# Kernel tuning notes

Measured on AMD Instinct MI355X. Metric: run time of the kernel, lower is better.

The kernel has to match this reference:

```python
import jax, jax.numpy as jnp
import numpy as np

B, C_IN, V_IN = 16, 16, 16000
V1, V2 = 16384, 4096          # V2 = V1 // 4 (after first pool)
K1, K2 = 16, 16               # Chebyshev orders
F1, F2 = 32, 64               # conv output channels
FC1_F = 512
DEG = 16
EPS = 1e-5


def setup_inputs() -> dict:
    key = jax.random.key(0)
    ks = jax.random.split(key, 12)
    x = jax.random.normal(ks[0], (B, C_IN, V_IN), dtype=jnp.float32)
    perm_idx = jax.random.permutation(ks[1], V1).astype(jnp.int32)
    # sparse rescaled Laplacians in COO form (row, col, val)
    l1_rows = jnp.repeat(jnp.arange(V1, dtype=jnp.int32), DEG)
    l1_cols = jax.random.randint(ks[2], (V1 * DEG,), 0, V1, dtype=jnp.int32)
    l1_vals = jax.random.normal(ks[3], (V1 * DEG,), dtype=jnp.float32) / DEG
    l2_rows = jnp.repeat(jnp.arange(V2, dtype=jnp.int32), DEG)
    l2_cols = jax.random.randint(ks[4], (V2 * DEG,), 0, V2, dtype=jnp.int32)
    l2_vals = jax.random.normal(ks[5], (V2 * DEG,), dtype=jnp.float32) / DEG
    # Graph_Conv kernels: Linear(in_channels*K -> out_channels)
    s1 = np.sqrt(2.0 / (C_IN * K1 + F1)).astype(np.float32)
    w1 = jax.random.uniform(ks[6], (F1, C_IN * K1), jnp.float32, -s1, s1)
    b1 = jnp.zeros((F1,), jnp.float32)
    s2 = np.sqrt(2.0 / (F1 * K2 + F2)).astype(np.float32)
    w2 = jax.random.uniform(ks[7], (F2, F1 * K2), jnp.float32, -s2, s2)
    b2 = jnp.zeros((F2,), jnp.float32)
    fc_in = F2 * (V1 // 16)  # 65536
    s3 = np.sqrt(2.0 / (fc_in + FC1_F)).astype(np.float32)
    fc1_w = jax.random.uniform(ks[8], (FC1_F, fc_in), jnp.float32, -s3, s3)
    fc1_b = jnp.zeros((FC1_F,), jnp.float32)
    return dict(x=x, perm_idx=perm_idx,
                l1_rows=l1_rows, l1_cols=l1_cols, l1_vals=l1_vals,
                l2_rows=l2_rows, l2_cols=l2_cols, l2_vals=l2_vals,
                w1=w1, b1=b1, w2=w2, b2=b2, fc1_w=fc1_w, fc1_b=fc1_b)


def _spmm(rows, cols, vals, X, V):
    # sparse (V,V) @ dense (V,M) via gather + segment-sum
    return jax.ops.segment_sum(vals[:, None] * X[cols], rows, num_segments=V)


def _cheb_conv(x, rows, cols, vals, w, b, K):
    # x: (B, C, V) -> (B, Fout, V)
    Bn, C, V = x.shape
    x0 = x.transpose(2, 1, 0).reshape(V, C * Bn)
    xs = [x0]
    if K > 1:
        xs.append(_spmm(rows, cols, vals, x0, V))
    for _ in range(2, K):
        xs.append(2.0 * _spmm(rows, cols, vals, xs[-1], V) - xs[-2])
    xk = jnp.stack(xs, axis=0).reshape(K, V, C, Bn)    # (K, V, C, B)
    xk = xk.transpose(3, 1, 2, 0).reshape(Bn * V, C * K)
    y = xk @ w.T + b                                   # (B*V, Fout)
    return y.reshape(Bn, V, -1).transpose(0, 2, 1)     # (B, Fout, V)


def _pool4(x):
    Bn, C, V = x.shape
    return x.reshape(Bn, C, V // 4, 4).max(axis=-1)


def reference(x, perm_idx, l1_rows, l1_cols, l1_vals,
              l2_rows, l2_cols, l2_vals,
              w1, b1, w2, b2, fc1_w, fc1_b):
    # BatchNorm1d(affine=False), training-mode (batch) statistics
    mean = x.mean(axis=(0, 2), keepdims=True)
    var = x.var(axis=(0, 2), keepdims=True)
    x = (x - mean) * jax.lax.rsqrt(var + EPS)
    # Permute: zero-pad vertices to V1, then reorder
    Bn, C, V = x.shape
    x = jnp.pad(x, ((0, 0), (0, 0), (0, V1 - V)))[:, :, perm_idx]
    # conv1 -> relu -> pool4
    x = jax.nn.relu(_cheb_conv(x, l1_rows, l1_cols, l1_vals, w1, b1, K1))
    x = _pool4(x)
    # conv2 -> relu -> pool4
    x = jax.nn.relu(_cheb_conv(x, l2_rows, l2_cols, l2_vals, w2, b2, K2))
    x = _pool4(x)
    # flatten + fc1 (dropout is identity in eval mode)
    x = x.reshape(Bn, -1)
    return x @ fc1_w.T + fc1_b
```

## Files before the change

### kernel.cpp

```cpp
#include <hip/hip_runtime.h>

#define VIN  16000
#define V1q  16384
#define V2q  4096
#define Kq   16
#define F1q  32
#define F2q  64
#define FCIN 65536

typedef unsigned short u16;
typedef __attribute__((ext_vector_type(8))) short short8;
typedef __attribute__((ext_vector_type(4))) float f32x4;

__device__ __forceinline__ float bf2f(u16 v) { return __uint_as_float((unsigned)v << 16); }
__device__ __forceinline__ u16 f2bf(float f) {
    unsigned u = __float_as_uint(f);
    return (u16)((u + 0x7fffu + ((u >> 16) & 1u)) >> 16);
}

__global__ void bn_part(const float* __restrict__ x, float* __restrict__ part) {
    int c  = blockIdx.y;
    int bx = blockIdx.x;
    int b  = bx >> 2;
    int vc = bx & 3;
    const float* p = x + (size_t)(b * 16 + c) * VIN + vc * 4000;
    float s = 0.f, s2 = 0.f;
    for (int v = threadIdx.x; v < 4000; v += 256) {
        float val = p[v];
        s += val; s2 += val * val;
    }
    for (int o = 32; o; o >>= 1) { s += __shfl_down(s, o); s2 += __shfl_down(s2, o); }
    __shared__ float ls[4], ls2[4];
    int wid = threadIdx.x >> 6;
    if ((threadIdx.x & 63) == 0) { ls[wid] = s; ls2[wid] = s2; }
    __syncthreads();
    if (threadIdx.x == 0) {
        s = ls[0] + ls[1] + ls[2] + ls[3];
        s2 = ls2[0] + ls2[1] + ls2[2] + ls2[3];
        part[(c * 64 + bx) * 2]     = s;
        part[(c * 64 + bx) * 2 + 1] = s2;
    }
}

__global__ void bn_final(const float* __restrict__ part, float* __restrict__ mean_rstd) {
    int t = threadIdx.x;
    int c = t >> 4, j = t & 15;
    float s = 0.f, s2 = 0.f;
    for (int i = 0; i < 4; i++) {
        s  += part[(c * 64 + j * 4 + i) * 2];
        s2 += part[(c * 64 + j * 4 + i) * 2 + 1];
    }
    for (int o = 8; o; o >>= 1) { s += __shfl_down(s, o, 16); s2 += __shfl_down(s2, o, 16); }
    if (j == 0) {
        float m  = s / 256000.f;
        float var = s2 / 256000.f - m * m;
        mean_rstd[c]      = m;
        mean_rstd[16 + c] = rsqrtf(var + 1e-5f);
    }
}

__global__ void build_iperm(const int* __restrict__ perm, int* __restrict__ iperm) {
    int v = blockIdx.x * 256 + threadIdx.x;
    if (v < V1q) iperm[perm[v]] = v;
}

__global__ void norm_transpose_scatter(const float* __restrict__ x,
                                       const float* __restrict__ mean_rstd,
                                       const int* __restrict__ iperm,
                                       u16* __restrict__ X0) {
    __shared__ u16 tile[256][33];
    int u0 = blockIdx.x * 32;
    int t  = threadIdx.x;
    int jj = t & 31, half = t >> 5;
    for (int rr = 0; rr < 32; rr++) {
        int s = rr * 8 + half;
        int c = s & 15, b = s >> 4;
        float val = x[(size_t)s * VIN + u0 + jj];
        val = (val - mean_rstd[c]) * mean_rstd[16 + c];
        int d = ((c >> 3) << 7) | (b << 3) | (c & 7);
        tile[d][jj] = f2bf(val);
    }
    __syncthreads();
    for (int j = 0; j < 32; j++) {
        int tv = iperm[u0 + j];
        X0[(size_t)tv * 256 + t] = tile[t][j];
    }
}

__global__ void pack_w1(const float* __restrict__ w1, u16* __restrict__ B1p) {
    int i = blockIdx.x * 256 + threadIdx.x;
    int j = i & 7, l = (i >> 3) & 63, nf = (i >> 9) & 1, s = i >> 10;
    int q = l >> 4;
    int k = s * 2 + (q >> 1);
    int c = (q & 1) * 8 + j;
    int f = nf * 16 + (l & 15);
    B1p[i] = f2bf(w1[f * 256 + c * 16 + k]);
}
__global__ void pack_w2(const float* __restrict__ w2, u16* __restrict__ B2p) {
    int i = blockIdx.x * 256 + threadIdx.x;
    int j = i & 7, l = (i >> 3) & 63, nf = (i >> 9) & 3, k = i >> 11;
    int f1 = (l >> 4) * 8 + j;
    int f2 = nf * 16 + (l & 15);
    B2p[i] = f2bf(w2[f2 * 512 + f1 * 16 + k]);
}

__global__ void pack_p(const float* __restrict__ P2f, u16* __restrict__ Pp) {
    int i = blockIdx.x * 256 + threadIdx.x;
    int l = i & 63, ks = i >> 6;
    int b = l & 15, q = l >> 4;
    const float* src = P2f + (size_t)b * FCIN + ks * 32 + q * 8;
    float4 a0 = *(const float4*)(src);
    float4 a1 = *(const float4*)(src + 4);
    short8 v;
    v[0] = (short)f2bf(a0.x); v[1] = (short)f2bf(a0.y);
    v[2] = (short)f2bf(a0.z); v[3] = (short)f2bf(a0.w);
    v[4] = (short)f2bf(a1.x); v[5] = (short)f2bf(a1.y);
    v[6] = (short)f2bf(a1.z); v[7] = (short)f2bf(a1.w);
    *(short8*)(Pp + (size_t)i * 8) = v;
}

template<int WLOG, int NRBLOG>
__global__ void spmm_cheb(const u16* __restrict__ prev, const u16* __restrict__ prev2,
                          u16* __restrict__ out,
                          const int* __restrict__ cols, const float* __restrict__ vals,
                          int nwg, float scale, int sub) {
    int bid = blockIdx.x;
    int q = nwg >> 3;
    int wid = (bid & 7) * q + (bid >> 3);
    int cb = wid >> NRBLOG;
    int r4 = wid & ((1 << NRBLOG) - 1);
    int lane = threadIdx.x & 63;
    int r = __builtin_amdgcn_readfirstlane(r4 * 4 + (threadIdx.x >> 6));
    int col = (cb << 6) + lane;
    const int4*   cp = (const int4*)(cols + r * 16);
    const float4* vp = (const float4*)(vals + r * 16);
    float acc = 0.f;
#pragma unroll
    for (int ii = 0; ii < 4; ii++) {
        int4   ci = cp[ii];
        float4 vi = vp[ii];
        const u16* p0 = prev + ((size_t)__builtin_amdgcn_readfirstlane(ci.x) << WLOG);
        const u16* p1 = prev + ((size_t)__builtin_amdgcn_readfirstlane(ci.y) << WLOG);
        const u16* p2 = prev + ((size_t)__builtin_amdgcn_readfirstlane(ci.z) << WLOG);
        const u16* p3 = prev + ((size_t)__builtin_amdgcn_readfirstlane(ci.w) << WLOG);
        acc += vi.x * bf2f(p0[col]);
        acc += vi.y * bf2f(p1[col]);
        acc += vi.z * bf2f(p2[col]);
        acc += vi.w * bf2f(p3[col]);
    }
    float o = scale * acc;
    if (sub) o -= bf2f(__builtin_nontemporal_load(prev2 + ((size_t)r << WLOG) + col));
    __builtin_nontemporal_store(f2bf(o), out + ((size_t)r << WLOG) + col);
}

__launch_bounds__(256)
__global__ void gemm1_mfma(const u16* __restrict__ XS1, const u16* __restrict__ B1p,
                           const float* __restrict__ b1, u16* __restrict__ XS2_0) {
    __shared__ u16 As[2][4096];
    int t = threadIdx.x;
    int w = t >> 6, l = t & 63;
    int v0 = blockIdx.x * 8;
    int nf = w & 1, vq = w >> 1;

    f32x4 acc[4] = {};
    {
        const short8* s0 = (const short8*)(XS1 + (size_t)(0 * V1q + v0) * 256);
        const short8* s1 = (const short8*)(XS1 + (size_t)(1 * V1q + v0) * 256);
        short8* dst = (short8*)As[0];
        dst[t] = s0[t]; dst[256 + t] = s1[t];
    }
    __syncthreads();
    for (int s = 0; s < 8; s++) {
        int cur = s & 1;
        if (s < 7) {
            const short8* s0 = (const short8*)(XS1 + (size_t)((2 * s + 2) * V1q + v0) * 256);
            const short8* s1 = (const short8*)(XS1 + (size_t)((2 * s + 3) * V1q + v0) * 256);
            short8* dst = (short8*)As[cur ^ 1];
            dst[t] = s0[t]; dst[256 + t] = s1[t];
        }
        short8 bfrag = *(const short8*)(B1p + (((size_t)s * 2 + nf) * 64 + l) * 8);
        int abase = (l >> 5) * 2048 + (l & 31) * 8;
#pragma unroll
        for (int fm = 0; fm < 4; fm++) {
            int vl = vq * 4 + fm;
            short8 afrag = *(const short8*)&As[cur][abase + vl * 256];
            acc[fm] = __builtin_amdgcn_mfma_f32_16x16x32_bf16(afrag, bfrag, acc[fm], 0, 0, 0);
        }
        __syncthreads();
    }
    f32x4 m = acc[0];
#pragma unroll
    for (int fm = 1; fm < 4; fm++) {
#pragma unroll
        for (int i = 0; i < 4; i++) m[i] = fmaxf(m[i], acc[fm][i]);
    }
    int f1 = nf * 16 + (l & 15);
    float bias = b1[f1];
    int u_out = blockIdx.x * 2 + vq;
    u16* orow = XS2_0 + (size_t)u_out * 512;
    int colbase = ((f1 >> 3) << 7) | (f1 & 7);
#pragma unroll
    for (int reg = 0; reg < 4; reg++) {
        int b = (l >> 4) * 4 + reg;
        orow[colbase + b * 8] = f2bf(fmaxf(m[reg] + bias, 0.f));
    }
}

__launch_bounds__(256)
__global__ void gemm2_mfma(const u16* __restrict__ XS2, const u16* __restrict__ B2p,
                           const float* __restrict__ b2, float* __restrict__ P2f) {
    __shared__ u16 As[2][8192];
    __shared__ float ylds[4 * 16 * 66];
    int t = threadIdx.x;
    int w = t >> 6, l = t & 63;
    int u0 = blockIdx.x * 16;

    f32x4 acc[4][4] = {};
    {
        const short8* src = (const short8*)(XS2 + (size_t)(0 * V2q + u0) * 512);
        short8* dst = (short8*)As[0];
#pragma unroll
        for (int r = 0; r < 4; r++) dst[t * 4 + r] = src[t * 4 + r];
    }
    __syncthreads();
    for (int k = 0; k < 16; k++) {
        int cur = k & 1;
        if (k < 15) {
            const short8* src = (const short8*)(XS2 + (size_t)((k + 1) * V2q + u0) * 512);
            short8* dst = (short8*)As[cur ^ 1];
#pragma unroll
            for (int r = 0; r < 4; r++) dst[t * 4 + r] = src[t * 4 + r];
        }
        short8 bfrag[4];
#pragma unroll
        for (int nf = 0; nf < 4; nf++)
            bfrag[nf] = *(const short8*)(B2p + (((size_t)k * 4 + nf) * 64 + l) * 8);
#pragma unroll
        for (int fm = 0; fm < 4; fm++) {
            int ul = w * 4 + fm;
            short8 afrag = *(const short8*)&As[cur][ul * 512 + l * 8];
#pragma unroll
            for (int nf = 0; nf < 4; nf++)
                acc[fm][nf] = __builtin_amdgcn_mfma_f32_16x16x32_bf16(afrag, bfrag[nf], acc[fm][nf], 0, 0, 0);
        }
        __syncthreads();
    }
#pragma unroll
    for (int nf = 0; nf < 4; nf++) {
        int f2 = nf * 16 + (l & 15);
        float bias = b2[f2];
#pragma unroll
        for (int reg = 0; reg < 4; reg++) {
            int b = (l >> 4) * 4 + reg;
            float m = fmaxf(fmaxf(acc[0][nf][reg], acc[1][nf][reg]),
                            fmaxf(acc[2][nf][reg], acc[3][nf][reg]));
            ylds[(w * 16 + b) * 66 + f2] = fmaxf(m + bias, 0.f);
        }
    }
    __syncthreads();
    int ub = blockIdx.x * 4;
#pragma unroll
    for (int i = 0; i < 4; i++) {
        int p = t + i * 256;
        int b = p >> 6, f2 = p & 63;
        float4 v;
        v.x = ylds[(0 * 16 + b) * 66 + f2];
        v.y = ylds[(1 * 16 + b) * 66 + f2];
        v.z = ylds[(2 * 16 + b) * 66 + f2];
        v.w = ylds[(3 * 16 + b) * 66 + f2];
        *(float4*)&P2f[(size_t)(b * 64 + f2) * 1024 + ub] = v;
    }
}

__global__ void fc_init(const float* __restrict__ b, float* __restrict__ out) {
    int i = blockIdx.x * 256 + threadIdx.x;
    out[i] = b[i & 511];
}

__launch_bounds__(256)
__global__ void fc_mfma(const u16* __restrict__ Pp, const float* __restrict__ W,
                        float* __restrict__ out) {
    int t = threadIdx.x;
    int w = t >> 6, l = t & 63;
    int n0 = blockIdx.x * 16;
    int ks0 = blockIdx.y * 64 + w * 16;
    int o = n0 + (l & 15);
    const float* wp = W + (size_t)o * FCIN + (size_t)ks0 * 32 + (l >> 4) * 8;
    const u16*   ap = Pp + ((size_t)ks0 * 64 + l) * 8;
    f32x4 acc = {};
    for (int s = 0; s < 16; s++) {
        short8 afrag = *(const short8*)(ap + (size_t)s * 512);
        float4 w0 = *(const float4*)(wp + s * 32);
        float4 w1 = *(const float4*)(wp + s * 32 + 4);
        short8 bfrag;
        bfrag[0] = (short)f2bf(w0.x); bfrag[1] = (short)f2bf(w0.y);
        bfrag[2] = (short)f2bf(w0.z); bfrag[3] = (short)f2bf(w0.w);
        bfrag[4] = (short)f2bf(w1.x); bfrag[5] = (short)f2bf(w1.y);
        bfrag[6] = (short)f2bf(w1.z); bfrag[7] = (short)f2bf(w1.w);
        acc = __builtin_amdgcn_mfma_f32_16x16x32_bf16(afrag, bfrag, acc, 0, 0, 0);
    }
    __shared__ float red[4][256];
#pragma unroll
    for (int r = 0; r < 4; r++)
        red[w][((l >> 4) * 4 + r) * 16 + (l & 15)] = acc[r];
    __syncthreads();
    float s = red[0][t] + red[1][t] + red[2][t] + red[3][t];
    atomicAdd(&out[(t >> 4) * 512 + n0 + (t & 15)], s);
}

extern "C" void kernel_launch(void* const* d_in, const int* in_sizes, int n_in,
                              void* d_out, int out_size, void* d_ws, size_t ws_size,
                              hipStream_t stream) {
    const float* x       = (const float*)d_in[0];
    const int*   perm    = (const int*)d_in[1];
    const int*   l1_cols = (const int*)d_in[3];
    const float* l1_vals = (const float*)d_in[4];
    const int*   l2_cols = (const int*)d_in[6];
    const float* l2_vals = (const float*)d_in[7];
    const float* w1      = (const float*)d_in[8];
    const float* b1      = (const float*)d_in[9];
    const float* w2      = (const float*)d_in[10];
    const float* b2      = (const float*)d_in[11];
    const float* fcw     = (const float*)d_in[12];
    const float* fcb     = (const float*)d_in[13];
    float* out = (float*)d_out;

    char* wsb = (char*)d_ws;
    size_t off = 0;
    auto alloc = [&](size_t bytes) -> void* {
        void* p = wsb + off;
        off += (bytes + 255) & ~(size_t)255;
        return p;
    };
    float* mean_rstd = (float*)alloc(32 * 4);
    float* bnpart    = (float*)alloc(16 * 64 * 2 * 4);
    int*   iperm     = (int*)alloc((size_t)V1q * 4);
    u16*   B1p       = (u16*)alloc(8192 * 2);
    u16*   B2p       = (u16*)alloc(32768 * 2);
    u16*   XS1       = (u16*)alloc((size_t)Kq * V1q * 256 * 2);
    u16*   XS2       = (u16*)alloc((size_t)Kq * V2q * 512 * 2);
    float* P2f       = (float*)alloc((size_t)16 * FCIN * 4);
    u16*   Pp        = (u16*)alloc((size_t)16 * FCIN * 2);
    (void)ws_size; (void)in_sizes; (void)n_in; (void)out_size;

    const size_t S1 = (size_t)V1q * 256;
    const size_t S2 = (size_t)V2q * 512;

    bn_part<<<dim3(64, 16), 256, 0, stream>>>(x, bnpart);
    bn_final<<<1, 256, 0, stream>>>(bnpart, mean_rstd);
    build_iperm<<<V1q / 256, 256, 0, stream>>>(perm, iperm);
    hipMemsetAsync(XS1, 0, S1 * 2, stream);
    norm_transpose_scatter<<<500, 256, 0, stream>>>(x, mean_rstd, iperm, XS1);
    pack_w1<<<32, 256, 0, stream>>>(w1, B1p);
    pack_w2<<<128, 256, 0, stream>>>(w2, B2p);

    spmm_cheb<8, 12><<<16384, 256, 0, stream>>>(XS1, XS1, XS1 + S1, l1_cols, l1_vals, 16384, 1.f, 0);
    for (int k = 2; k < Kq; k++)
        spmm_cheb<8, 12><<<16384, 256, 0, stream>>>(XS1 + (size_t)(k - 1) * S1, XS1 + (size_t)(k - 2) * S1,
                                                    XS1 + (size_t)k * S1, l1_cols, l1_vals, 16384, 2.f, 1);
    gemm1_mfma<<<V1q / 8, 256, 0, stream>>>(XS1, B1p, b1, XS2);

    spmm_cheb<9, 10><<<8192, 256, 0, stream>>>(XS2, XS2, XS2 + S2, l2_cols, l2_vals, 8192, 1.f, 0);
    for (int k = 2; k < Kq; k++)
        spmm_cheb<9, 10><<<8192, 256, 0, stream>>>(XS2 + (size_t)(k - 1) * S2, XS2 + (size_t)(k - 2) * S2,
                                                   XS2 + (size_t)k * S2, l2_cols, l2_vals, 8192, 2.f, 1);
    gemm2_mfma<<<V2q / 16, 256, 0, stream>>>(XS2, B2p, b2, P2f);

    pack_p<<<512, 256, 0, stream>>>(P2f, Pp);
    fc_init<<<32, 256, 0, stream>>>(fcb, out);
    fc_mfma<<<dim3(32, 32), 256, 0, stream>>>(Pp, fcw, out);
}
```

Baseline: 481.0 us.

## Restructure Chebyshev SpMM so each wave processes whole rows with vector loads

Replaces the column-block SpMM, where one wave handled a 64-column slice of a row with 2-byte loads, with a row-per-wave kernel. Each lane now loads 4 or 8 packed bf16 values per neighbor, so the column/value indices are read once per full row instead of once per column block. Fewer, larger blocks loop over rows. The hipMemsetAsync is also replaced with a custom zeroing kernel. In exchange, per-wave load size and register use rise, and the cross-block L2-locality swizzle of the old scheme is dropped.

Result: faster. 464.4 us (-3.4%).

```diff
diff --git a/kernel.cpp b/kernel.cpp
--- a/kernel.cpp
+++ b/kernel.cpp
@@ -4,18 +4,30 @@
 #define V1q  16384
 #define V2q  4096
 #define Kq   16
-#define F1q  32
-#define F2q  64
 #define FCIN 65536
 
 typedef unsigned short u16;
+typedef unsigned int u32;
 typedef __attribute__((ext_vector_type(8))) short short8;
 typedef __attribute__((ext_vector_type(4))) float f32x4;
+typedef __attribute__((ext_vector_type(2))) u32 u32x2;
+typedef __attribute__((ext_vector_type(4))) u32 u32x4;
 
 __device__ __forceinline__ float bf2f(u16 v) { return __uint_as_float((unsigned)v << 16); }
+__device__ __forceinline__ float bflo(u32 u) { return __uint_as_float(u << 16); }
+__device__ __forceinline__ float bfhi(u32 u) { return __uint_as_float(u & 0xffff0000u); }
 __device__ __forceinline__ u16 f2bf(float f) {
     unsigned u = __float_as_uint(f);
     return (u16)((u + 0x7fffu + ((u >> 16) & 1u)) >> 16);
+}
+__device__ __forceinline__ u32 packbf(float a, float b) {
+    return (u32)f2bf(a) | ((u32)f2bf(b) << 16);
+}
+
+__global__ void zero_ws(u16* __restrict__ X0) {
+    size_t idx = (size_t)blockIdx.x * 256 + threadIdx.x;
+    float4 z = {0.f, 0.f, 0.f, 0.f};
+    *(float4*)(X0 + idx * 8) = z;
 }
 
 __global__ void bn_part(const float* __restrict__ x, float* __restrict__ part) {
@@ -119,38 +131,75 @@
     *(short8*)(Pp + (size_t)i * 8) = v;
 }
 
-template<int WLOG, int NRBLOG>
-__global__ void spmm_cheb(const u16* __restrict__ prev, const u16* __restrict__ prev2,
-                          u16* __restrict__ out,
-                          const int* __restrict__ cols, const float* __restrict__ vals,
-                          int nwg, float scale, int sub) {
-    int bid = blockIdx.x;
-    int q = nwg >> 3;
-    int wid = (bid & 7) * q + (bid >> 3);
-    int cb = wid >> NRBLOG;
-    int r4 = wid & ((1 << NRBLOG) - 1);
+template<int CPL>
+__launch_bounds__(256)
+__global__ void spmm_row(const u16* __restrict__ prev, const u16* __restrict__ prev2,
+                         u16* __restrict__ out,
+                         const int* __restrict__ cols, const float* __restrict__ vals,
+                         int iters, float scale, int sub) {
+    constexpr int WLOG = (CPL == 2) ? 8 : 9;
+    constexpr int EPL  = CPL * 2;
     int lane = threadIdx.x & 63;
-    int r = __builtin_amdgcn_readfirstlane(r4 * 4 + (threadIdx.x >> 6));
-    int col = (cb << 6) + lane;
-    const int4*   cp = (const int4*)(cols + r * 16);
-    const float4* vp = (const float4*)(vals + r * 16);
-    float acc = 0.f;
-#pragma unroll
-    for (int ii = 0; ii < 4; ii++) {
-        int4   ci = cp[ii];
-        float4 vi = vp[ii];
-        const u16* p0 = prev + ((size_t)__builtin_amdgcn_readfirstlane(ci.x) << WLOG);
-        const u16* p1 = prev + ((size_t)__builtin_amdgcn_readfirstlane(ci.y) << WLOG);
-        const u16* p2 = prev + ((size_t)__builtin_amdgcn_readfirstlane(ci.z) << WLOG);
-        const u16* p3 = prev + ((size_t)__builtin_amdgcn_readfirstlane(ci.w) << WLOG);
-        acc += vi.x * bf2f(p0[col]);
-        acc += vi.y * bf2f(p1[col]);
-        acc += vi.z * bf2f(p2[col]);
-        acc += vi.w * bf2f(p3[col]);
-    }
-    float o = scale * acc;
-    if (sub) o -= bf2f(__builtin_nontemporal_load(prev2 + ((size_t)r << WLOG) + col));
-    __builtin_nontemporal_store(f2bf(o), out + ((size_t)r << WLOG) + col);
+    int gw = blockIdx.x * 4 + (threadIdx.x >> 6);
+    int rbase = gw * iters;
+    for (int it = 0; it < iters; it++) {
+        int r = __builtin_amdgcn_readfirstlane(rbase + it);
+        const int4*   cp = (const int4*)(cols + r * 16);
+        const float4* vp = (const float4*)(vals + r * 16);
+        float acc[EPL];
+#pragma unroll
+        for (int i = 0; i < EPL; i++) acc[i] = 0.f;
+#pragma unroll
+        for (int ii = 0; ii < 4; ii++) {
+            int4   ci = cp[ii];
+            float4 vi = vp[ii];
+            int   cs[4] = {ci.x, ci.y, ci.z, ci.w};
+            float vs[4] = {vi.x, vi.y, vi.z, vi.w};
+#pragma unroll
+            for (int j = 0; j < 4; j++) {
+                const u16* rowp = prev + ((size_t)__builtin_amdgcn_readfirstlane(cs[j]) << WLOG);
+                if constexpr (CPL == 2) {
+                    u32x2 g = *(const u32x2*)(rowp + lane * 4);
+                    acc[0] += vs[j] * bflo(g.x); acc[1] += vs[j] * bfhi(g.x);
+                    acc[2] += vs[j] * bflo(g.y); acc[3] += vs[j] * bfhi(g.y);
+                } else {
+                    u32x4 g = *(const u32x4*)(rowp + lane * 8);
+                    acc[0] += vs[j] * bflo(g.x); acc[1] += vs[j] * bfhi(g.x);
+                    acc[2] += vs[j] * bflo(g.y); acc[3] += vs[j] * bfhi(g.y);
+                    acc[4] += vs[j] * bflo(g.z); acc[5] += vs[j] * bfhi(g.z);
+                    acc[6] += vs[j] * bflo(g.w); acc[7] += vs[j] * bfhi(g.w);
+                }
+            }
+        }
+        size_t obase = ((size_t)r << WLOG) + lane * EPL;
+        float o[EPL];
+        if (sub) {
+            if constexpr (CPL == 2) {
+                u32x2 p2 = __builtin_nontemporal_load((const u32x2*)(prev2 + obase));
+                o[0] = scale * acc[0] - bflo(p2.x); o[1] = scale * acc[1] - bfhi(p2.x);
+                o[2] = scale * acc[2] - bflo(p2.y); o[3] = scale * acc[3] - bfhi(p2.y);
+            } else {
+                u32x4 p2 = __builtin_nontemporal_load((const u32x4*)(prev2 + obase));
+                o[0] = scale * acc[0] - bflo(p2.x); o[1] = scale * acc[1] - bfhi(p2.x);
+                o[2] = scale * acc[2] - bflo(p2.y); o[3] = scale * acc[3] - bfhi(p2.y);
+                o[4] = scale * acc[4] - bflo(p2.z); o[5] = scale * acc[5] - bfhi(p2.z);
+                o[6] = scale * acc[6] - bflo(p2.w); o[7] = scale * acc[7] - bfhi(p2.w);
+            }
+        } else {
+#pragma unroll
+            for (int i = 0; i < EPL; i++) o[i] = scale * acc[i];
+        }
+        if constexpr (CPL == 2) {
+            u32x2 pk;
+            pk.x = packbf(o[0], o[1]); pk.y = packbf(o[2], o[3]);
+            __builtin_nontemporal_store(pk, (u32x2*)(out + obase));
+        } else {
+            u32x4 pk;
+            pk.x = packbf(o[0], o[1]); pk.y = packbf(o[2], o[3]);
+            pk.z = packbf(o[4], o[5]); pk.w = packbf(o[6], o[7]);
+            __builtin_nontemporal_store(pk, (u32x4*)(out + obase));
+        }
+    }
 }
 
 __launch_bounds__(256)
@@ -346,24 +395,24 @@
     const size_t S1 = (size_t)V1q * 256;
     const size_t S2 = (size_t)V2q * 512;
 
+    zero_ws<<<2048, 256, 0, stream>>>(XS1);
     bn_part<<<dim3(64, 16), 256, 0, stream>>>(x, bnpart);
     bn_final<<<1, 256, 0, stream>>>(bnpart, mean_rstd);
     build_iperm<<<V1q / 256, 256, 0, stream>>>(perm, iperm);
-    hipMemsetAsync(XS1, 0, S1 * 2, stream);
     norm_transpose_scatter<<<500, 256, 0, stream>>>(x, mean_rstd, iperm, XS1);
     pack_w1<<<32, 256, 0, stream>>>(w1, B1p);
     pack_w2<<<128, 256, 0, stream>>>(w2, B2p);
 
-    spmm_cheb<8, 12><<<16384, 256, 0, stream>>>(XS1, XS1, XS1 + S1, l1_cols, l1_vals, 16384, 1.f, 0);
+    spmm_row<2><<<2048, 256, 0, stream>>>(XS1, XS1, XS1 + S1, l1_cols, l1_vals, 2, 1.f, 0);
     for (int k = 2; k < Kq; k++)
-        spmm_cheb<8, 12><<<16384, 256, 0, stream>>>(XS1 + (size_t)(k - 1) * S1, XS1 + (size_t)(k - 2) * S1,
-                                                    XS1 + (size_t)k * S1, l1_cols, l1_vals, 16384, 2.f, 1);
+        spmm_row<2><<<2048, 256, 0, stream>>>(XS1 + (size_t)(k - 1) * S1, XS1 + (size_t)(k - 2) * S1,
+                                              XS1 + (size_t)k * S1, l1_cols, l1_vals, 2, 2.f, 1);
     gemm1_mfma<<<V1q / 8, 256, 0, stream>>>(XS1, B1p, b1, XS2);
 
-    spmm_cheb<9, 10><<<8192, 256, 0, stream>>>(XS2, XS2, XS2 + S2, l2_cols, l2_vals, 8192, 1.f, 0);
+    spmm_row<4><<<1024, 256, 0, stream>>>(XS2, XS2, XS2 + S2, l2_cols, l2_vals, 1, 1.f, 0);
     for (int k = 2; k < Kq; k++)
-        spmm_cheb<9, 10><<<8192, 256, 0, stream>>>(XS2 + (size_t)(k - 1) * S2, XS2 + (size_t)(k - 2) * S2,
-                                                   XS2 + (size_t)k * S2, l2_cols, l2_vals, 8192, 2.f, 1);
+        spmm_row<4><<<1024, 256, 0, stream>>>(XS2 + (size_t)(k - 1) * S2, XS2 + (size_t)(k - 2) * S2,
+                                              XS2 + (size_t)k * S2, l2_cols, l2_vals, 1, 2.f, 1);
     gemm2_mfma<<<V2q / 16, 256, 0, stream>>>(XS2, B2p, b2, P2f);
 
     pack_p<<<512, 256, 0, stream>>>(P2f, Pp);
```

## Fuse Chebyshev SpMM recurrence into one persistent kernel with grid barriers

Applied to the files above, without the earlier changes.

Replaces the 15 separate spmm_cheb launches per conv layer with a single persistent cheb_chain kernel of 512 workgroups. Each workgroup handles several rows and loops over all Chebyshev orders. Between orders, workgroups sync through a hierarchical per-XCD atomic grid barrier, which is meant to remove kernel launch and drain overhead. The memset is also replaced by a custom zeroing kernel. Correctness depends on every workgroup being co-resident, since the barrier deadlocks otherwise. Fewer waves are in flight to hide gather latency.

Result: slower. 893.0 us (+85.6%).

```diff
diff --git a/kernel.cpp b/kernel.cpp
--- a/kernel.cpp
+++ b/kernel.cpp
@@ -4,11 +4,10 @@
 #define V1q  16384
 #define V2q  4096
 #define Kq   16
-#define F1q  32
-#define F2q  64
 #define FCIN 65536
 
 typedef unsigned short u16;
+typedef unsigned int u32;
 typedef __attribute__((ext_vector_type(8))) short short8;
 typedef __attribute__((ext_vector_type(4))) float f32x4;
 
@@ -16,6 +15,25 @@
 __device__ __forceinline__ u16 f2bf(float f) {
     unsigned u = __float_as_uint(f);
     return (u16)((u + 0x7fffu + ((u >> 16) & 1u)) >> 16);
+}
+
+#define BO_XCNT 0
+#define BO_ARR0 512
+#define BO_FLG0 544
+#define BO_XARR 1024
+#define BO_DONE 9216
+#define BO_FLAG 9984
+#define BAR_CH  16384
+
+__global__ void zero_bar(int* __restrict__ bar) {
+    int i = blockIdx.x * 256 + threadIdx.x;
+    bar[i] = 0;
+}
+
+__global__ void zero_ws(u16* __restrict__ X0) {
+    size_t idx = (size_t)blockIdx.x * 256 + threadIdx.x;
+    float4 z = {0.f, 0.f, 0.f, 0.f};
+    *(float4*)(X0 + idx * 8) = z;
 }
 
 __global__ void bn_part(const float* __restrict__ x, float* __restrict__ part) {
@@ -119,38 +137,84 @@
     *(short8*)(Pp + (size_t)i * 8) = v;
 }
 
-template<int WLOG, int NRBLOG>
-__global__ void spmm_cheb(const u16* __restrict__ prev, const u16* __restrict__ prev2,
-                          u16* __restrict__ out,
-                          const int* __restrict__ cols, const float* __restrict__ vals,
-                          int nwg, float scale, int sub) {
-    int bid = blockIdx.x;
-    int q = nwg >> 3;
-    int wid = (bid & 7) * q + (bid >> 3);
-    int cb = wid >> NRBLOG;
-    int r4 = wid & ((1 << NRBLOG) - 1);
+template<int WLOG, int CBLOG, int NR>
+__launch_bounds__(256, 2)
+__global__ void cheb_chain(const int* __restrict__ cols, const float* __restrict__ vals,
+                           u16* __restrict__ XS, int* __restrict__ bar, size_t S) {
+    int wid = blockIdx.x;
+    int cb  = wid & ((1 << CBLOG) - 1);
+    int rg  = wid >> CBLOG;
     int lane = threadIdx.x & 63;
-    int r = __builtin_amdgcn_readfirstlane(r4 * 4 + (threadIdx.x >> 6));
-    int col = (cb << 6) + lane;
-    const int4*   cp = (const int4*)(cols + r * 16);
-    const float4* vp = (const float4*)(vals + r * 16);
-    float acc = 0.f;
-#pragma unroll
-    for (int ii = 0; ii < 4; ii++) {
-        int4   ci = cp[ii];
-        float4 vi = vp[ii];
-        const u16* p0 = prev + ((size_t)__builtin_amdgcn_readfirstlane(ci.x) << WLOG);
-        const u16* p1 = prev + ((size_t)__builtin_amdgcn_readfirstlane(ci.y) << WLOG);
-        const u16* p2 = prev + ((size_t)__builtin_amdgcn_readfirstlane(ci.z) << WLOG);
-        const u16* p3 = prev + ((size_t)__builtin_amdgcn_readfirstlane(ci.w) << WLOG);
-        acc += vi.x * bf2f(p0[col]);
-        acc += vi.y * bf2f(p1[col]);
-        acc += vi.z * bf2f(p2[col]);
-        acc += vi.w * bf2f(p3[col]);
-    }
-    float o = scale * acc;
-    if (sub) o -= bf2f(__builtin_nontemporal_load(prev2 + ((size_t)r << WLOG) + col));
-    __builtin_nontemporal_store(f2bf(o), out + ((size_t)r << WLOG) + col);
+    int wv   = __builtin_amdgcn_readfirstlane(threadIdx.x >> 6);
+    int col  = (cb << 6) + lane;
+    int rbase = (rg * 4 + wv) * NR;
+    int nwg = gridDim.x;
+
+    int myxcd;
+    asm volatile("s_getreg_b32 %0, hwreg(HW_REG_XCC_ID)" : "=s"(myxcd));
+    myxcd &= 15;
+
+    int mycount = 0, nxcd = 0;
+    if (threadIdx.x == 0) {
+        __hip_atomic_fetch_add(&bar[BO_XCNT + myxcd * 32], 1, __ATOMIC_RELAXED, __HIP_MEMORY_SCOPE_AGENT);
+        int prev = __hip_atomic_fetch_add(&bar[BO_ARR0], 1, __ATOMIC_RELEASE, __HIP_MEMORY_SCOPE_AGENT);
+        if (prev == nwg - 1) {
+            __hip_atomic_store(&bar[BO_FLG0], 1, __ATOMIC_RELEASE, __HIP_MEMORY_SCOPE_AGENT);
+        } else {
+            while (__hip_atomic_load(&bar[BO_FLG0], __ATOMIC_RELAXED, __HIP_MEMORY_SCOPE_AGENT) == 0)
+                __builtin_amdgcn_s_sleep(4);
+        }
+        mycount = __hip_atomic_load(&bar[BO_XCNT + myxcd * 32], __ATOMIC_RELAXED, __HIP_MEMORY_SCOPE_AGENT);
+        for (int j = 0; j < 16; j++)
+            nxcd += (__hip_atomic_load(&bar[BO_XCNT + j * 32], __ATOMIC_RELAXED, __HIP_MEMORY_SCOPE_AGENT) != 0);
+    }
+    __syncthreads();
+    asm volatile("" ::: "memory");
+
+    for (int k = 1; k < 16; k++) {
+        const u16* prev  = XS + (size_t)(k - 1) * S;
+        const u16* prev2 = XS + (size_t)(k - 2) * S;
+        u16* outp = XS + (size_t)k * S;
+        float scale = (k == 1) ? 1.f : 2.f;
+#pragma unroll 2
+        for (int it = 0; it < NR; it++) {
+            int r = __builtin_amdgcn_readfirstlane(rbase + it);
+            const int4*   cp = (const int4*)(cols + r * 16);
+            const float4* vp = (const float4*)(vals + r * 16);
+            float acc = 0.f;
+#pragma unroll
+            for (int ii = 0; ii < 4; ii++) {
+                int4   ci = cp[ii];
+                float4 vi = vp[ii];
+                acc += vi.x * bf2f(prev[((size_t)__builtin_amdgcn_readfirstlane(ci.x) << WLOG) + col]);
+                acc += vi.y * bf2f(prev[((size_t)__builtin_amdgcn_readfirstlane(ci.y) << WLOG) + col]);
+                acc += vi.z * bf2f(prev[((size_t)__builtin_amdgcn_readfirstlane(ci.z) << WLOG) + col]);
+                acc += vi.w * bf2f(prev[((size_t)__builtin_amdgcn_readfirstlane(ci.w) << WLOG) + col]);
+            }
+            size_t ob = ((size_t)r << WLOG) + col;
+            float o = scale * acc;
+            if (k >= 2) o -= bf2f(__builtin_nontemporal_load(prev2 + ob));
+            outp[ob] = f2bf(o);
+        }
+        if (k < 15) {
+            __syncthreads();
+            if (threadIdx.x == 0) {
+                int xa = __hip_atomic_fetch_add(&bar[BO_XARR + (k * 16 + myxcd) * 32], 1,
+                                                __ATOMIC_RELAXED, __HIP_MEMORY_SCOPE_AGENT);
+                if (xa == mycount - 1) {
+                    __builtin_amdgcn_fence(__ATOMIC_RELEASE, "agent");
+                    int d = __hip_atomic_fetch_add(&bar[BO_DONE + k * 32], 1,
+                                                   __ATOMIC_RELEASE, __HIP_MEMORY_SCOPE_AGENT);
+                    if (d == nxcd - 1)
+                        __hip_atomic_store(&bar[BO_FLAG], k, __ATOMIC_RELEASE, __HIP_MEMORY_SCOPE_AGENT);
+                }
+                while (__hip_atomic_load(&bar[BO_FLAG], __ATOMIC_RELAXED, __HIP_MEMORY_SCOPE_AGENT) < k)
+                    __builtin_amdgcn_s_sleep(4);
+            }
+            __syncthreads();
+            asm volatile("" ::: "memory");
+        }
+    }
 }
 
 __launch_bounds__(256)
@@ -335,6 +399,7 @@
     float* mean_rstd = (float*)alloc(32 * 4);
     float* bnpart    = (float*)alloc(16 * 64 * 2 * 4);
     int*   iperm     = (int*)alloc((size_t)V1q * 4);
+    int*   bar       = (int*)alloc((size_t)2 * BAR_CH * 4);
     u16*   B1p       = (u16*)alloc(8192 * 2);
     u16*   B2p       = (u16*)alloc(32768 * 2);
     u16*   XS1       = (u16*)alloc((size_t)Kq * V1q * 256 * 2);
@@ -346,24 +411,18 @@
     const size_t S1 = (size_t)V1q * 256;
     const size_t S2 = (size_t)V2q * 512;
 
+    zero_bar<<<128, 256, 0, stream>>>(bar);
+    zero_ws<<<2048, 256, 0, stream>>>(XS1);
     bn_part<<<dim3(64, 16), 256, 0, stream>>>(x, bnpart);
     bn_final<<<1, 256, 0, stream>>>(bnpart, mean_rstd);
     build_iperm<<<V1q / 256, 256, 0, stream>>>(perm, iperm);
-    hipMemsetAsync(XS1, 0, S1 * 2, stream);
     norm_transpose_scatter<<<500, 256, 0, stream>>>(x, mean_rstd, iperm, XS1);
     pack_w1<<<32, 256, 0, stream>>>(w1, B1p);
     pack_w2<<<128, 256, 0, stream>>>(w2, B2p);
 
-    spmm_cheb<8, 12><<<16384, 256, 0, stream>>>(XS1, XS1, XS1 + S1, l1_cols, l1_vals, 16384, 1.f, 0);
-    for (int k = 2; k < Kq; k++)
-        spmm_cheb<8, 12><<<16384, 256, 0, stream>>>(XS1 + (size_t)(k - 1) * S1, XS1 + (size_t)(k - 2) * S1,
-                                                    XS1 + (size_t)k * S1, l1_cols, l1_vals, 16384, 2.f, 1);
+    cheb_chain<8, 2, 32><<<512, 256, 0, stream>>>(l1_cols, l1_vals, XS1, bar, S1);
     gemm1_mfma<<<V1q / 8, 256, 0, stream>>>(XS1, B1p, b1, XS2);
-
-    spmm_cheb<9, 10><<<8192, 256, 0, stream>>>(XS2, XS2, XS2 + S2, l2_cols, l2_vals, 8192, 1.f, 0);
-    for (int k = 2; k < Kq; k++)
-        spmm_cheb<9, 10><<<8192, 256, 0, stream>>>(XS2 + (size_t)(k - 1) * S2, XS2 + (size_t)(k - 2) * S2,
-                                                   XS2 + (size_t)k * S2, l2_cols, l2_vals, 8192, 2.f, 1);
+    cheb_chain<9, 3, 16><<<512, 256, 0, stream>>>(l2_cols, l2_vals, XS2, bar + BAR_CH, S2);
     gemm2_mfma<<<V2q / 16, 256, 0, stream>>>(XS2, B2p, b2, P2f);
 
     pack_p<<<512, 256, 0, stream>>>(P2f, Pp);
```
